# Performance work log

Hardware: AMD Instinct MI355X
Metric: run time of the kernel (lower is better)

Reference implementation:

```python
import jax, jax.numpy as jnp
import numpy as np

GMIN, GMAX = 0.1, 1.0
DIMS = [3, 256, 256, 256, 1]

def setup_inputs() -> dict:
    key = jax.random.key(0)
    ks = jax.random.split(key, 12)
    inp = {"pos": jax.random.normal(ks[0], (1048576, 3), dtype=jnp.float32)}
    for i in range(4):
        fan_in = DIMS[i]
        bound = 1.0 / np.sqrt(fan_in)
        inp[f"W{i}"] = jax.random.uniform(ks[1 + 2 * i], (fan_in, DIMS[i + 1]), jnp.float32, -bound, bound)
        inp[f"b{i}"] = jax.random.uniform(ks[2 + 2 * i], (DIMS[i + 1],), jnp.float32, -bound, bound)
    for i in range(3):
        inp[f"sigma{i}"] = jax.random.uniform(ks[9 + i], (256,), jnp.float32, GMIN, GMAX)
    return inp

def _gauss(x, sigma):
    # Gaussian activation: exp(-x^2 / (2*sigma^2)), sigma learnable per-feature
    return jnp.exp(-jnp.square(x) / (2.0 * jnp.square(sigma)))

def _softplus8(x):
    # torch Softplus(beta=1, threshold=8): linear beyond threshold
    return jnp.where(x > 8.0, x, jnp.log1p(jnp.exp(jnp.minimum(x, 8.0))))

def reference(pos, W0, b0, W1, b1, W2, b2, W3, b3, sigma0, sigma1, sigma2):
    h = _gauss(pos @ W0 + b0, sigma0)      # [N,256]
    h = _gauss(h @ W1 + b1, sigma1)        # [N,256]
    h = _gauss(h @ W2 + b2, sigma2)        # [N,256]
    return _softplus8(h @ W3 + b3)         # [N,1]
```

## Files before the change

kernel.cpp:

```cpp
#include <hip/hip_runtime.h>
#include <hip/hip_bf16.h>

typedef __attribute__((ext_vector_type(8))) short short8;
typedef __attribute__((ext_vector_type(4))) float f32x4;
typedef __attribute__((ext_vector_type(2))) float f32x2;
typedef __attribute__((ext_vector_type(2))) unsigned int uint2v;
typedef __attribute__((ext_vector_type(4))) unsigned int u32x4;

#define LOG2E 1.4426950408889634f
#define LN2   0.6931471805599453f

__device__ __forceinline__ unsigned short f2bf(float f) {
    union { float f; unsigned u; } v; v.f = f;
    unsigned u = v.u;
    u += 0x7fffu + ((u >> 16) & 1u);
    return (unsigned short)(u >> 16);
}
__device__ __forceinline__ float bf2f(unsigned short h) {
    union { unsigned u; float f; } v; v.u = ((unsigned)h) << 16;
    return v.f;
}
__device__ __forceinline__ float bitf(unsigned u) {
    union { unsigned u; float f; } v; v.u = u;
    return v.f;
}
__device__ __forceinline__ unsigned pk_bf16(float a, float b) {
    __hip_bfloat162 t = __float22bfloat162_rn(float2{a, b});
    union { __hip_bfloat162 b; unsigned u; } v; v.b = t;
    return v.u;
}
__device__ __forceinline__ f32x2 pk_fma2(f32x2 a, f32x2 b, f32x2 c) {
    f32x2 d;
    asm("v_pk_fma_f32 %0, %1, %2, %3" : "=v"(d) : "v"(a), "v"(b), "v"(c));
    return d;
}

__global__ void pack_kernel(const float* __restrict__ W0, const float* __restrict__ W1,
                            const float* __restrict__ W2,
                            const float* __restrict__ s0, const float* __restrict__ s1,
                            const float* __restrict__ s2,
                            const float* __restrict__ b0, const float* __restrict__ b1,
                            const float* __restrict__ b2,
                            unsigned short* __restrict__ wp, float* __restrict__ negc) {
    int tid = blockIdx.x * 256 + threadIdx.x;
    if (tid < 8192) {
        int j = tid & 7, lane = (tid >> 3) & 63, ct = (tid >> 9) & 3, w = tid >> 11;
        int k = ((lane >> 4) * 8) + j;
        int n = w * 64 + 4 * (lane & 15) + ct;
        unsigned short v = 0;
        if (k < 9) {
            int d = k / 3, m = k - d * 3;
            float wv = W0[d * 256 + n];
            unsigned short wh = f2bf(wv);
            v = (m == 1) ? f2bf(wv - bf2f(wh)) : wh;
        }
        wp[tid] = v;
    } else if (tid < 139264) {
        int e = tid - 8192;
        const float* W = W1;
        if (e >= 65536) { W = W2; e -= 65536; }
        int j = e & 7, lane = (e >> 3) & 63, ct = (e >> 9) & 3, ks = (e >> 11) & 7, w = e >> 14;
        int k = ks * 32 + ((lane >> 4) * 8) + j;
        int n = w * 64 + 4 * (lane & 15) + ct;
        wp[tid] = f2bf(W[k * 256 + n]);
    }
    if (tid < 768) {
        int l = tid >> 8, n = tid & 255;
        const float* s = (l == 0) ? s0 : (l == 1 ? s1 : s2);
        const float* b = (l == 0) ? b0 : (l == 1 ? b1 : b2);
        float sv = s[n], bv = b[n];
        float np = -LOG2E / (2.0f * sv * sv);
        negc[l * 768 + n]       = np;
        negc[l * 768 + 256 + n] = 2.0f * np * bv;
        negc[l * 768 + 512 + n] = np * bv * bv;
    }
}

constexpr int ROWS = 64;
constexpr int HSTR = 264;
constexpr int ASTR = 40;

template <int NKS, int SSTR>
__device__ __forceinline__ void layer(const unsigned short* __restrict__ src,
                                      const unsigned short* __restrict__ wpk,
                                      const float* __restrict__ ncp,
                                      unsigned short* __restrict__ hdst,
                                      int w, int i16, int q, bool presync) {
    f32x4 acc[4][4];
#pragma unroll
    for (int rg = 0; rg < 4; ++rg)
#pragma unroll
        for (int ct = 0; ct < 4; ++ct)
            acc[rg][ct] = f32x4{0.f, 0.f, 0.f, 0.f};

    const int lane = q * 16 + i16;
    const short8* wp8 = (const short8*)wpk + (w * NKS * 4) * 64 + lane;
    const unsigned short* abase = src + i16 * SSTR + q * 8;

#pragma unroll
    for (int ks = 0; ks < NKS; ++ks) {
        short8 a[4];
#pragma unroll
        for (int rg = 0; rg < 4; ++rg)
            a[rg] = *(const short8*)(abase + rg * 16 * SSTR + ks * 32);
#pragma unroll
        for (int ct = 0; ct < 4; ++ct) {
            short8 wf = wp8[(ks * 4 + ct) * 64];
#pragma unroll
            for (int rg = 0; rg < 4; ++rg)
                acc[rg][ct] = __builtin_amdgcn_mfma_f32_16x16x32_bf16(a[rg], wf, acc[rg][ct], 0, 0, 0);
        }
    }

    const int ce = w * 64 + 4 * i16;
    const f32x4 np = *(const f32x4*)(ncp + ce);
    const f32x4 C1 = *(const f32x4*)(ncp + 256 + ce);
    const f32x4 C2 = *(const f32x4*)(ncp + 512 + ce);
    f32x2 npb[4], c1b[4], c2b[4];
#pragma unroll
    for (int ct = 0; ct < 4; ++ct) {
        npb[ct] = f32x2{np[ct], np[ct]};
        c1b[ct] = f32x2{C1[ct], C1[ct]};
        c2b[ct] = f32x2{C2[ct], C2[ct]};
    }
    uint2v av[4][4];
#pragma unroll
    for (int rg = 0; rg < 4; ++rg) {
        float gg[4][4];
#pragma unroll
        for (int ct = 0; ct < 4; ++ct) {
            f32x2 xlo = f32x2{acc[rg][ct][0], acc[rg][ct][1]};
            f32x2 xhi = f32x2{acc[rg][ct][2], acc[rg][ct][3]};
            f32x2 ulo = pk_fma2(npb[ct], xlo, c1b[ct]);
            f32x2 uhi = pk_fma2(npb[ct], xhi, c1b[ct]);
            f32x2 ylo = pk_fma2(ulo, xlo, c2b[ct]);
            f32x2 yhi = pk_fma2(uhi, xhi, c2b[ct]);
            gg[0][ct] = __builtin_amdgcn_exp2f(ylo[0]);
            gg[1][ct] = __builtin_amdgcn_exp2f(ylo[1]);
            gg[2][ct] = __builtin_amdgcn_exp2f(yhi[0]);
            gg[3][ct] = __builtin_amdgcn_exp2f(yhi[1]);
        }
#pragma unroll
        for (int rr = 0; rr < 4; ++rr) {
            uint2v v;
            v[0] = pk_bf16(gg[rr][0], gg[rr][1]);
            v[1] = pk_bf16(gg[rr][2], gg[rr][3]);
            av[rg][rr] = v;
        }
    }
    if (presync) __syncthreads();
#pragma unroll
    for (int rg = 0; rg < 4; ++rg) {
        int rbase = rg * 16 + q * 4;
#pragma unroll
        for (int rr = 0; rr < 4; ++rr)
            *(uint2v*)&hdst[(rbase + rr) * HSTR + ce] = av[rg][rr];
    }
    __syncthreads();
}

__global__ __launch_bounds__(256, 3) void mlp_kernel(
    const float* __restrict__ pos,
    const float* __restrict__ W3, const float* __restrict__ b3,
    const unsigned short* __restrict__ Wp,
    const float* __restrict__ negc,
    float* __restrict__ out)
{
    __shared__ unsigned short h[ROWS * HSTR];
    __shared__ unsigned short A0[ROWS * ASTR];

    const int tid  = threadIdx.x;
    const int lane = tid & 63;
    const int wave = tid >> 6;
    const int i16  = lane & 15, q = lane >> 4;
    const long row0 = (long)blockIdx.x * ROWS;

    if (tid < ROWS) {
        const float* pp = pos + (row0 + tid) * 3;
        float p0 = pp[0], p1 = pp[1], p2 = pp[2];
        short h0 = (short)f2bf(p0); short l0 = (short)f2bf(p0 - bf2f((unsigned short)h0));
        short h1 = (short)f2bf(p1); short l1 = (short)f2bf(p1 - bf2f((unsigned short)h1));
        short h2 = (short)f2bf(p2); short l2 = (short)f2bf(p2 - bf2f((unsigned short)h2));
        unsigned short* arow = A0 + tid * ASTR;
        *(short8*)(arow + 0)  = short8{h0, h0, l0, h1, h1, l1, h2, h2};
        *(short8*)(arow + 8)  = short8{l2, 0, 0, 0, 0, 0, 0, 0};
        *(short8*)(arow + 16) = short8{0, 0, 0, 0, 0, 0, 0, 0};
        *(short8*)(arow + 24) = short8{0, 0, 0, 0, 0, 0, 0, 0};
    }
    __syncthreads();

    layer<1, ASTR>(A0, Wp,         negc,        h, wave, i16, q, false);
    layer<8, HSTR>(h,  Wp + 8192,  negc + 768,  h, wave, i16, q, true);
    layer<8, HSTR>(h,  Wp + 73728, negc + 1536, h, wave, i16, q, true);

    {
        int r = tid >> 2, qq = tid & 3;
        const unsigned short* hrow = h + r * HSTR;
        f32x2 sa = {0.f, 0.f}, sb = {0.f, 0.f};
#pragma unroll
        for (int i = 0; i < 8; ++i) {
            int c = (qq + 4 * i) * 8;
            u32x4 hv = *(const u32x4*)(hrow + c);
            f32x4 wA = *(const f32x4*)(W3 + c);
            f32x4 wB = *(const f32x4*)(W3 + c + 4);
            f32x2 p0 = f32x2{bitf(hv[0] << 16), bitf(hv[0] & 0xffff0000u)};
            f32x2 p1 = f32x2{bitf(hv[1] << 16), bitf(hv[1] & 0xffff0000u)};
            f32x2 p2 = f32x2{bitf(hv[2] << 16), bitf(hv[2] & 0xffff0000u)};
            f32x2 p3 = f32x2{bitf(hv[3] << 16), bitf(hv[3] & 0xffff0000u)};
            sa = pk_fma2(p0, f32x2{wA[0], wA[1]}, sa);
            sb = pk_fma2(p1, f32x2{wA[2], wA[3]}, sb);
            sa = pk_fma2(p2, f32x2{wB[0], wB[1]}, sa);
            sb = pk_fma2(p3, f32x2{wB[2], wB[3]}, sb);
        }
        float s = sa[0] + sa[1] + sb[0] + sb[1];
        s += __shfl_xor(s, 1);
        s += __shfl_xor(s, 2);
        if (qq == 0) {
            float x  = s + b3[0];
            float xm = fminf(x, 8.0f);
            float e  = __builtin_amdgcn_exp2f(xm * LOG2E);
            float sp = __builtin_amdgcn_logf(1.0f + e) * LN2;
            out[row0 + r] = (x > 8.0f) ? x : sp;
        }
    }
}

extern "C" void kernel_launch(void* const* d_in, const int* in_sizes, int n_in,
                              void* d_out, int out_size, void* d_ws, size_t ws_size,
                              hipStream_t stream) {
    const float* pos = (const float*)d_in[0];
    const float* W0  = (const float*)d_in[1];
    const float* b0  = (const float*)d_in[2];
    const float* W1  = (const float*)d_in[3];
    const float* b1  = (const float*)d_in[4];
    const float* W2  = (const float*)d_in[5];
    const float* b2  = (const float*)d_in[6];
    const float* W3  = (const float*)d_in[7];
    const float* b3  = (const float*)d_in[8];
    const float* s0  = (const float*)d_in[9];
    const float* s1  = (const float*)d_in[10];
    const float* s2  = (const float*)d_in[11];

    unsigned short* wp = (unsigned short*)d_ws;
    float* negc = (float*)((char*)d_ws + 278528);

    pack_kernel<<<544, 256, 0, stream>>>(W0, W1, W2, s0, s1, s2, b0, b1, b2, wp, negc);

    int nrows = in_sizes[0] / 3;
    int nblk  = nrows / ROWS;
    mlp_kernel<<<nblk, 256, 0, stream>>>(pos, W3, b3, wp, negc,
                                         (float*)d_out);
}
```

Measured before the change: 411.5 us.

## Compute final layer with split-bf16 MFMA and double-buffer weight fragment loads

The final 256-to-1 projection, previously scalar packed FMAs per row, now runs on MFMA. W3 is pre-packed as a hi/lo bf16 split in two columns of a 16-wide tile, and each wave reduces its 64-column slice. Partial sums go through shared scratch (reusing A0) and one extra barrier before a single thread per row sums them and applies softplus. Separately, the per-k-step weight fragment loads in the layer loop are prefetched one step ahead into alternating register buffers to hide global load latency, at the cost of higher register pressure.

```diff
diff --git a/kernel.cpp b/kernel.cpp
--- a/kernel.cpp
+++ b/kernel.cpp
@@ -5,7 +5,6 @@
 typedef __attribute__((ext_vector_type(4))) float f32x4;
 typedef __attribute__((ext_vector_type(2))) float f32x2;
 typedef __attribute__((ext_vector_type(2))) unsigned int uint2v;
-typedef __attribute__((ext_vector_type(4))) unsigned int u32x4;
 
 #define LOG2E 1.4426950408889634f
 #define LN2   0.6931471805599453f
@@ -20,10 +19,6 @@
     union { unsigned u; float f; } v; v.u = ((unsigned)h) << 16;
     return v.f;
 }
-__device__ __forceinline__ float bitf(unsigned u) {
-    union { unsigned u; float f; } v; v.u = u;
-    return v.f;
-}
 __device__ __forceinline__ unsigned pk_bf16(float a, float b) {
     __hip_bfloat162 t = __float22bfloat162_rn(float2{a, b});
     union { __hip_bfloat162 b; unsigned u; } v; v.b = t;
@@ -36,7 +31,7 @@
 }
 
 __global__ void pack_kernel(const float* __restrict__ W0, const float* __restrict__ W1,
-                            const float* __restrict__ W2,
+                            const float* __restrict__ W2, const float* __restrict__ W3,
                             const float* __restrict__ s0, const float* __restrict__ s1,
                             const float* __restrict__ s2,
                             const float* __restrict__ b0, const float* __restrict__ b1,
@@ -63,6 +58,17 @@
         int k = ks * 32 + ((lane >> 4) * 8) + j;
         int n = w * 64 + 4 * (lane & 15) + ct;
         wp[tid] = f2bf(W[k * 256 + n]);
+    } else if (tid < 143360) {
+        int e = tid - 139264;
+        int j = e & 7, lane = (e >> 3) & 63, ks = (e >> 9) & 1, w = e >> 10;
+        int i16p = lane & 15, qp = lane >> 4;
+        int k = w * 64 + ks * 32 + qp * 8 + j;
+        float wv = W3[k];
+        unsigned short wh = f2bf(wv);
+        unsigned short v = 0;
+        if (i16p == 0) v = wh;
+        else if (i16p == 1) v = f2bf(wv - bf2f(wh));
+        wp[139264 + e] = v;
     }
     if (tid < 768) {
         int l = tid >> 8, n = tid & 255;
@@ -97,15 +103,26 @@
     const short8* wp8 = (const short8*)wpk + (w * NKS * 4) * 64 + lane;
     const unsigned short* abase = src + i16 * SSTR + q * 8;
 
+    short8 wbufA[4], wbufB[4];
+#pragma unroll
+    for (int ct = 0; ct < 4; ++ct) wbufA[ct] = wp8[ct * 64];
+
 #pragma unroll
     for (int ks = 0; ks < NKS; ++ks) {
+        if (ks + 1 < NKS) {
+#pragma unroll
+            for (int ct = 0; ct < 4; ++ct) {
+                short8 t = wp8[((ks + 1) * 4 + ct) * 64];
+                if (ks & 1) wbufA[ct] = t; else wbufB[ct] = t;
+            }
+        }
         short8 a[4];
 #pragma unroll
         for (int rg = 0; rg < 4; ++rg)
             a[rg] = *(const short8*)(abase + rg * 16 * SSTR + ks * 32);
 #pragma unroll
         for (int ct = 0; ct < 4; ++ct) {
-            short8 wf = wp8[(ks * 4 + ct) * 64];
+            short8 wf = (ks & 1) ? wbufB[ct] : wbufA[ct];
 #pragma unroll
             for (int rg = 0; rg < 4; ++rg)
                 acc[rg][ct] = __builtin_amdgcn_mfma_f32_16x16x32_bf16(a[rg], wf, acc[rg][ct], 0, 0, 0);
@@ -161,7 +178,7 @@
 
 __global__ __launch_bounds__(256, 3) void mlp_kernel(
     const float* __restrict__ pos,
-    const float* __restrict__ W3, const float* __restrict__ b3,
+    const float* __restrict__ b3,
     const unsigned short* __restrict__ Wp,
     const float* __restrict__ negc,
     float* __restrict__ out)
@@ -194,33 +211,36 @@
     layer<8, HSTR>(h,  Wp + 73728, negc + 1536, h, wave, i16, q, true);
 
     {
-        int r = tid >> 2, qq = tid & 3;
-        const unsigned short* hrow = h + r * HSTR;
-        f32x2 sa = {0.f, 0.f}, sb = {0.f, 0.f};
-#pragma unroll
-        for (int i = 0; i < 8; ++i) {
-            int c = (qq + 4 * i) * 8;
-            u32x4 hv = *(const u32x4*)(hrow + c);
-            f32x4 wA = *(const f32x4*)(W3 + c);
-            f32x4 wB = *(const f32x4*)(W3 + c + 4);
-            f32x2 p0 = f32x2{bitf(hv[0] << 16), bitf(hv[0] & 0xffff0000u)};
-            f32x2 p1 = f32x2{bitf(hv[1] << 16), bitf(hv[1] & 0xffff0000u)};
-            f32x2 p2 = f32x2{bitf(hv[2] << 16), bitf(hv[2] & 0xffff0000u)};
-            f32x2 p3 = f32x2{bitf(hv[3] << 16), bitf(hv[3] & 0xffff0000u)};
-            sa = pk_fma2(p0, f32x2{wA[0], wA[1]}, sa);
-            sb = pk_fma2(p1, f32x2{wA[2], wA[3]}, sb);
-            sa = pk_fma2(p2, f32x2{wB[0], wB[1]}, sa);
-            sb = pk_fma2(p3, f32x2{wB[2], wB[3]}, sb);
-        }
-        float s = sa[0] + sa[1] + sb[0] + sb[1];
-        s += __shfl_xor(s, 1);
-        s += __shfl_xor(s, 2);
-        if (qq == 0) {
+        const short8* w3p = (const short8*)(Wp + 139264) + (wave * 2) * 64 + lane;
+        const unsigned short* ab3 = h + i16 * HSTR + wave * 64 + q * 8;
+        f32x4 acc3[4];
+#pragma unroll
+        for (int rg = 0; rg < 4; ++rg) acc3[rg] = f32x4{0.f, 0.f, 0.f, 0.f};
+#pragma unroll
+        for (int ks = 0; ks < 2; ++ks) {
+            short8 wf = w3p[ks * 64];
+#pragma unroll
+            for (int rg = 0; rg < 4; ++rg) {
+                short8 a = *(const short8*)(ab3 + rg * 16 * HSTR + ks * 32);
+                acc3[rg] = __builtin_amdgcn_mfma_f32_16x16x32_bf16(a, wf, acc3[rg], 0, 0, 0);
+            }
+        }
+        float* scr = (float*)A0;
+        if (i16 < 2) {
+#pragma unroll
+            for (int rg = 0; rg < 4; ++rg)
+                *(f32x4*)&scr[(wave * 2 + i16) * 64 + rg * 16 + q * 4] = acc3[rg];
+        }
+        __syncthreads();
+        if (tid < 64) {
+            float s = 0.f;
+#pragma unroll
+            for (int g = 0; g < 8; ++g) s += scr[g * 64 + tid];
             float x  = s + b3[0];
             float xm = fminf(x, 8.0f);
             float e  = __builtin_amdgcn_exp2f(xm * LOG2E);
             float sp = __builtin_amdgcn_logf(1.0f + e) * LN2;
-            out[row0 + r] = (x > 8.0f) ? x : sp;
+            out[row0 + tid] = (x > 8.0f) ? x : sp;
         }
     }
 }
@@ -242,12 +262,12 @@
     const float* s2  = (const float*)d_in[11];
 
     unsigned short* wp = (unsigned short*)d_ws;
-    float* negc = (float*)((char*)d_ws + 278528);
-
-    pack_kernel<<<544, 256, 0, stream>>>(W0, W1, W2, s0, s1, s2, b0, b1, b2, wp, negc);
+    float* negc = (float*)((char*)d_ws + 286720);
+
+    pack_kernel<<<560, 256, 0, stream>>>(W0, W1, W2, W3, s0, s1, s2, b0, b1, b2, wp, negc);
 
     int nrows = in_sizes[0] / 3;
     int nblk  = nrows / ROWS;
-    mlp_kernel<<<nblk, 256, 0, stream>>>(pos, W3, b3, wp, negc,
+    mlp_kernel<<<nblk, 256, 0, stream>>>(pos, b3, wp, negc,
                                          (float*)d_out);
 }
```

Result: faster. 400.3 us (-2.7%).
